# Performance work log

Measured on AMD Instinct MI355X. Metric: run time of the kernel, lower is better.

The kernel has to match this reference:

```python
import jax, jax.numpy as jnp
import numpy as np

N = 100_000          # nodes
E = 3_200_000        # edges (avg degree 32)
NEG_SLOPE = 0.2      # PyG GATConv default


def _gat_conv(x, src, dst, W, a_src, a_dst, b, n):
    """Single-head PyG-style GATConv. src/dst already include self-loops."""
    h = x @ W                                   # [N, F_out]
    logits = (h @ a_src)[src] + (h @ a_dst)[dst]  # [E']
    e = jax.nn.leaky_relu(logits, NEG_SLOPE)
    m = jax.ops.segment_max(e, dst, num_segments=n)
    ex = jnp.exp(e - m[dst])                    # stable ragged softmax over in-edges
    s = jax.ops.segment_sum(ex, dst, num_segments=n)
    alpha = ex / (s[dst] + 1e-16)
    out = jax.ops.segment_sum(h[src] * alpha[:, None], dst, num_segments=n)
    return out + b


def setup_inputs() -> dict:
    key = jax.random.key(0)
    ks = jax.random.split(key, 20)
    x = jax.random.normal(ks[0], (N, 3), dtype=jnp.float32)
    edge_index = jax.random.randint(ks[1], (2, E), 0, N, dtype=jnp.int64)

    def lin(k, fin, fout):
        return jax.random.normal(k, (fin, fout), dtype=jnp.float32) * (1.0 / np.sqrt(fin))

    def att(k, f):
        return jax.random.normal(k, (f,), dtype=jnp.float32) * (1.0 / np.sqrt(f))

    inp = {"x": x, "edge_index": edge_index}
    # forward-direction convs
    inp["W1"], inp["as1"], inp["ad1"], inp["b1"] = lin(ks[2], 3, 16), att(ks[3], 16), att(ks[4], 16), jnp.zeros((16,), jnp.float32)
    inp["W2"], inp["as2"], inp["ad2"], inp["b2"] = lin(ks[5], 16, 1), att(ks[6], 1), att(ks[7], 1), jnp.zeros((1,), jnp.float32)
    # reverse-direction convs
    inp["W1r"], inp["as1r"], inp["ad1r"], inp["b1r"] = lin(ks[8], 3, 16), att(ks[9], 16), att(ks[10], 16), jnp.zeros((16,), jnp.float32)
    inp["W2r"], inp["as2r"], inp["ad2r"], inp["b2r"] = lin(ks[11], 16, 1), att(ks[12], 1), att(ks[13], 1), jnp.zeros((1,), jnp.float32)
    return inp


def reference(x, edge_index, W1, as1, ad1, b1, W2, as2, ad2, b2,
              W1r, as1r, ad1r, b1r, W2r, as2r, ad2r, b2r):
    n = x.shape[0]
    loops = jnp.arange(n, dtype=edge_index.dtype)
    # forward direction (self-loops appended, as PyG add_self_loops=True)
    src = jnp.concatenate([edge_index[0], loops])
    dst = jnp.concatenate([edge_index[1], loops])
    # reverse direction: stack([ei[1], ei[0]]) then self-loops
    rsrc = jnp.concatenate([edge_index[1], loops])
    rdst = jnp.concatenate([edge_index[0], loops])

    xf = jax.nn.relu(_gat_conv(x, src, dst, W1, as1, ad1, b1, n))
    xf = _gat_conv(xf, src, dst, W2, as2, ad2, b2, n)

    xr = jax.nn.relu(_gat_conv(x, rsrc, rdst, W1r, as1r, ad1r, b1r, n))
    xr = _gat_conv(xr, rsrc, rdst, W2r, as2r, ad2r, b2r, n)

    return (xf + xr) * 0.5
```

## Files before the change

kernel.cpp:

```cpp
#include <hip/hip_runtime.h>
#include <math.h>

#define NSLOPE 0.2f
#define BSH 8
#define BNODES 256
#define NID_MASK 0x1FFFF
#define SENT 0xFFFFFFFFu
#define CAP 10240
#define GB2 512
#define RT 512
#define EPT2 13
#define REDG (RT * EPT2)
#define RREC (2 * REDG)
#define BN9 512
#define LCAP 17408
#define BAGT 1024
#define CPP9 9

__device__ __forceinline__ float lrelu(float v) { return v > 0.f ? v : NSLOPE * v; }

__global__ void k_prep(const float* __restrict__ x,
                       const float* __restrict__ as1, const float* __restrict__ ad1,
                       const float* __restrict__ as1r, const float* __restrict__ ad1r,
                       const float* __restrict__ W1, const float* __restrict__ W1r,
                       float4* __restrict__ rec4f, float4* __restrict__ rec4r,
                       float* __restrict__ s1df, float* __restrict__ s1dr,
                       int* __restrict__ gcur, int NS, int N) {
    int i = blockIdx.x * blockDim.x + threadIdx.x;
    if (i < NS) gcur[i] = 0;
    if (i >= N) return;
    float x0 = x[3 * i], x1 = x[3 * i + 1], x2 = x[3 * i + 2];
    float ssf = 0.f, sdf = 0.f, ssr = 0.f, sdr = 0.f;
#pragma unroll
    for (int k = 0; k < 16; k++) {
        float hf = x0 * W1[k] + x1 * W1[16 + k] + x2 * W1[32 + k];
        ssf += hf * as1[k];
        sdf += hf * ad1[k];
        float hr = x0 * W1r[k] + x1 * W1r[16 + k] + x2 * W1r[32 + k];
        ssr += hr * as1r[k];
        sdr += hr * ad1r[k];
    }
    rec4f[i] = make_float4(x0, x1, x2, ssf);
    rec4r[i] = make_float4(x0, x1, x2, ssr);
    s1df[i] = sdf; s1dr[i] = sdr;
}

__global__ void __launch_bounds__(RT) k_scatsort(
        const void* __restrict__ ei, long long E,
        int NB, int NS, int* __restrict__ gcur, unsigned* __restrict__ bin) {
    extern __shared__ unsigned smem[];
    unsigned* rec = smem;
    int* cnt  = (int*)(rec + RREC);
    int* loff = cnt + NS;
    int* gbs  = loff + NS;
    int* wtot = gbs + NS;
    __shared__ int flagsm;

    int t = threadIdx.x;
    if (t < 64) {
        const unsigned long long* p = (const unsigned long long*)ei;
        bool bad = false;
#pragma unroll
        for (int i = 0; i < 4; i++)
            if (p[t * 4 + i] >= (1ull << 32)) bad = true;
        unsigned long long mask = __ballot(bad);
        if (t == 0) flagsm = (mask == 0ull) ? 1 : 0;
    }
    __syncthreads();
    int fl = flagsm;
    long long chunk = (E + GB2 - 1) / GB2;
    long long cstart = (long long)blockIdx.x * chunk;
    long long cend = cstart + chunk; if (cend > E) cend = E;
    int rot = (int)((blockIdx.x * 197u) % (unsigned)NS);

    for (long long rs = cstart; rs < cend; rs += REDG) {
        int ne = (int)min((long long)REDG, cend - rs);
        for (int i = t; i < NS; i += RT) cnt[i] = 0;
        int eu[EPT2], ev[EPT2];
#pragma unroll
        for (int k = 0; k < EPT2; k++) {
            int idx = t + k * RT;
            eu[k] = -1;
            if (idx < ne) {
                long long i = rs + idx;
                if (fl) { const long long* p = (const long long*)ei;
                          eu[k] = (int)p[i]; ev[k] = (int)p[E + i]; }
                else    { const int* p = (const int*)ei;
                          eu[k] = p[i]; ev[k] = p[E + i]; }
            }
        }
        __syncthreads();
#pragma unroll
        for (int k = 0; k < EPT2; k++) {
            if (eu[k] >= 0) {
                atomicAdd(&cnt[ev[k] >> BSH], 1);
                atomicAdd(&cnt[NB + (eu[k] >> BSH)], 1);
            }
        }
        __syncthreads();
        int base = 0;
        for (int st = 0; st < NS; st += RT) {
            int idx = st + t;
            int val = (idx < NS) ? cnt[idx] : 0;
            int lane = t & 63, wv = t >> 6;
            int incl = val;
#pragma unroll
            for (int od = 1; od < 64; od <<= 1) {
                int up = __shfl_up(incl, od);
                if (lane >= od) incl += up;
            }
            if (lane == 63) wtot[wv] = incl;
            __syncthreads();
            int woff = 0;
#pragma unroll
            for (int j = 0; j < 8; j++) woff += (j < wv) ? wtot[j] : 0;
            if (idx < NS) {
                int lo = base + woff + incl - val;
                loff[idx] = lo;
                cnt[idx] = lo;
                gbs[idx] = val ? atomicAdd(&gcur[idx], val) : 0;
            }
            int stot = 0;
#pragma unroll
            for (int j = 0; j < 8; j++) stot += wtot[j];
            base += stot;
            __syncthreads();
        }
#pragma unroll
        for (int k = 0; k < EPT2; k++) {
            if (eu[k] >= 0) {
                int u = eu[k], v = ev[k];
                unsigned r0 = (unsigned)u | ((unsigned)(v & (BNODES - 1)) << 17);
                int s0 = v >> BSH;
                int p0 = atomicAdd(&cnt[s0], 1);
                rec[p0] = r0;
                unsigned r1 = (unsigned)v | ((unsigned)(u & (BNODES - 1)) << 17);
                int s1 = NB + (u >> BSH);
                int p1 = atomicAdd(&cnt[s1], 1);
                rec[p1] = r1;
            }
        }
        __syncthreads();
        for (int i = t; i < NS; i += RT) {
            int s = i + rot; if (s >= NS) s -= NS;
            int ls = loff[s], le = cnt[s];
            int n = le - ls;
            if (!n) continue;
            int g = gbs[s];
            if (g >= CAP) continue;
            if (g + n > CAP) n = CAP - g;
            long long b = (long long)s * CAP;
            int j = 0;
            if (g & 1) { bin[b + g] = rec[ls]; j = 1; }
            if (((g + j) & 2) && j + 2 <= n) {
                *(uint2*)(bin + b + g + j) = make_uint2(rec[ls + j], rec[ls + j + 1]);
                j += 2;
            }
            for (; j + 4 <= n; j += 4)
                *(uint4*)(bin + b + g + j) =
                    make_uint4(rec[ls + j], rec[ls + j + 1],
                               rec[ls + j + 2], rec[ls + j + 3]);
            if (j + 2 <= n) {
                *(uint2*)(bin + b + g + j) = make_uint2(rec[ls + j], rec[ls + j + 1]);
                j += 2;
            }
            if (j < n) bin[b + g + j] = rec[ls + j];
        }
        __syncthreads();
    }
}

__global__ void __launch_bounds__(BAGT, 8) k_bagg1(
        unsigned* __restrict__ bin, const int* __restrict__ gcur,
        const float4* __restrict__ rec4f, const float* __restrict__ s1df,
        const float4* __restrict__ rec4r, const float* __restrict__ s1dr,
        const float* __restrict__ b1, const float* __restrict__ W1,
        const float* __restrict__ W2,
        const float* __restrict__ as2, const float* __restrict__ ad2,
        const float* __restrict__ b1r, const float* __restrict__ W1r,
        const float* __restrict__ W2r,
        const float* __restrict__ as2r, const float* __restrict__ ad2r,
        float2* __restrict__ p2f, float* __restrict__ s2df,
        float2* __restrict__ p2r, float* __restrict__ s2dr,
        int* __restrict__ aoff, int* __restrict__ aend, int NB8, int N) {
    int bb = blockIdx.x, dir = blockIdx.y;
    const float4* rec4 = dir ? rec4r : rec4f;
    const float* s1d = dir ? s1dr : s1df;
    const float* b1_ = dir ? b1r : b1;
    const float* W1_ = dir ? W1r : W1;
    const float* W2_ = dir ? W2r : W2;
    float as2v = dir ? as2r[0] : as2[0];
    float ad2v = dir ? ad2r[0] : ad2[0];
    float2* p2 = dir ? p2r : p2f;
    float* s2d = dir ? s2dr : s2df;

    int c0 = dir * NB8 + 2 * bb;
    bool c1ok = (2 * bb + 1) < NB8;
    long long base = (long long)c0 * CAP;
    int n0 = gcur[c0]; if (n0 > CAP) n0 = CAP;
    int n1 = c1ok ? gcur[c0 + 1] : 0; if (n1 > CAP) n1 = CAP;
    int np0 = (n0 + 1) >> 1, np1 = (n1 + 1) >> 1;
    if (np0 > LCAP / 2) np0 = LCAP / 2;
    if (np0 + np1 > LCAP / 2) np1 = LCAP / 2 - np0;
    int nptot = np0 + np1;
    int v0 = bb << 9;
    int nv = N - v0; if (nv > BN9) nv = BN9;

    __shared__ int cnt[BN9];
    __shared__ int loff[BN9];
    __shared__ int segtot[8];
    __shared__ unsigned lds_u[LCAP];
    int t = threadIdx.x;

    const uint2* bp0 = (const uint2*)(bin + base);
    const uint2* bp1 = (const uint2*)(bin + base) + CAP / 2;
    uint2 recs[CPP9];
#pragma unroll
    for (int k = 0; k < CPP9; k++) {
        int i = t + k * BAGT;
        uint2 r = make_uint2(SENT, SENT);
        if (i < np0) {
            r = bp0[i];
            if (2 * i + 1 >= n0) r.y = SENT;
        } else if (i < nptot) {
            int i1 = i - np0;
            r = bp1[i1];
            if (2 * i1 + 1 >= n1) r.y = SENT;
            r.x += (256u << 17);
            if (r.y != SENT) r.y += (256u << 17);
        }
        recs[k] = r;
    }
    if (t < BN9) cnt[t] = 0;
    __syncthreads();
#pragma unroll
    for (int k = 0; k < CPP9; k++) {
        if (recs[k].x != SENT) atomicAdd(&cnt[recs[k].x >> 17], 1);
        if (recs[k].y != SENT) atomicAdd(&cnt[recs[k].y >> 17], 1);
    }
    __syncthreads();
    if (t < BN9) {
        int lane = t & 63, wv = t >> 6;
        int val = cnt[t];
        int incl = val;
#pragma unroll
        for (int od = 1; od < 64; od <<= 1) {
            int up = __shfl_up(incl, od);
            if (lane >= od) incl += up;
        }
        if (lane == 63) segtot[wv] = incl;
        loff[t] = incl - val;
    }
    __syncthreads();
    if (t < BN9) {
        int wv = t >> 6;
        int offs = 0;
#pragma unroll
        for (int j = 0; j < 8; j++) offs += (j < wv) ? segtot[j] : 0;
        int ex = loff[t] + offs;
        loff[t] = ex;
        cnt[t] = ex;
    }
    __syncthreads();
#pragma unroll
    for (int k = 0; k < CPP9; k++) {
        if (recs[k].x != SENT) {
            int q = atomicAdd(&cnt[recs[k].x >> 17], 1);
            lds_u[q] = recs[k].x & NID_MASK;
        }
        if (recs[k].y != SENT) {
            int q = atomicAdd(&cnt[recs[k].y >> 17], 1);
            lds_u[q] = recs[k].y & NID_MASK;
        }
    }
    __syncthreads();
    int node = t >> 1, lane = t & 1;
    float sdv = (node < nv) ? s1d[v0 + node] : 0.f;
    float d = 0.f, a0 = 0.f, a1 = 0.f, a2 = 0.f;
    if (node < nv) {
        int ls = loff[node], le = cnt[node];
        for (int pos = ls + lane; pos < le; pos += 2) {
            unsigned u = lds_u[pos];
            float4 r = rec4[u];
            float w = __expf(lrelu(r.w + sdv));
            d += w; a0 += w * r.x; a1 += w * r.y; a2 += w * r.z;
        }
    }
    d  += __shfl_xor(d, 1);
    a0 += __shfl_xor(a0, 1);
    a1 += __shfl_xor(a1, 1);
    a2 += __shfl_xor(a2, 1);
    if (lane == 0 && node < nv) {
        int v = v0 + node;
        float4 r = rec4[v];
        float w = __expf(lrelu(r.w + sdv));
        float dd = d + w;
        float inv = 1.f / (dd + 1e-16f);
        float m0 = (a0 + w * r.x) * inv;
        float m1 = (a1 + w * r.y) * inv;
        float m2 = (a2 + w * r.z) * inv;
        float h2v = 0.f;
#pragma unroll
        for (int k = 0; k < 16; k++) {
            float o = m0 * W1_[k] + m1 * W1_[16 + k] + m2 * W1_[32 + k] + b1_[k];
            o = fmaxf(o, 0.f);
            h2v += o * W2_[k];
        }
        p2[v] = make_float2(h2v, h2v * as2v);
        s2d[v] = h2v * ad2v;
    }
    int nreal = (nv > 0) ? cnt[nv - 1] : 0;
    if (t == 0 && (nreal & 1)) lds_u[nreal] = SENT;
    __syncthreads();
    int ndp = (nreal + 1) >> 1;
    uint2* bq = (uint2*)(bin + base);
    for (int i = t; i < ndp; i += BAGT)
        bq[i] = make_uint2(lds_u[2 * i], lds_u[2 * i + 1]);
    if (t < nv) {
        aoff[dir * N + v0 + t] = (int)(base + loff[t]);
        aend[dir * N + v0 + t] = (int)(base + cnt[t]);
    }
}

__global__ void k_agg2(const unsigned* __restrict__ bin,
                       const int* __restrict__ aoff, const int* __restrict__ aend,
                       const float2* __restrict__ p2f, const float* __restrict__ s2df,
                       const float2* __restrict__ p2r, const float* __restrict__ s2dr,
                       const float* __restrict__ b2, const float* __restrict__ b2r,
                       float* __restrict__ out, int N) {
    int tid = blockIdx.x * blockDim.x + threadIdx.x;
    int v = tid >> 4;
    int lane = tid & 15;
    if (v >= N) return;
    float res[2];
#pragma unroll
    for (int dir = 0; dir < 2; dir++) {
        const float2* p2 = dir ? p2r : p2f;
        const float* s2d = dir ? s2dr : s2df;
        float bias = dir ? b2r[0] : b2[0];
        float sd = s2d[v];
        int st = aoff[dir * N + v], en = aend[dir * N + v];
        float d = 0.f, a = 0.f;
        if (lane == 0) {
            float2 ts = p2[v];
            float w = __expf(lrelu(ts.y + sd));
            d = w; a = w * ts.x;
        }
        int j = st + lane;
        for (; j + 16 < en; j += 32) {
            unsigned u0 = __builtin_nontemporal_load(bin + j);
            unsigned u1 = __builtin_nontemporal_load(bin + j + 16);
            float2 t0 = p2[u0];
            float2 t1 = p2[u1];
            float w0 = __expf(lrelu(t0.y + sd));
            float w1 = __expf(lrelu(t1.y + sd));
            d += w0 + w1;
            a += w0 * t0.x + w1 * t1.x;
        }
        for (; j < en; j += 16) {
            unsigned u = __builtin_nontemporal_load(bin + j);
            float2 t = p2[u];
            float w = __expf(lrelu(t.y + sd));
            d += w;
            a += w * t.x;
        }
#pragma unroll
        for (int mask = 1; mask < 16; mask <<= 1) {
            d += __shfl_xor(d, mask);
            a += __shfl_xor(a, mask);
        }
        res[dir] = a / (d + 1e-16f) + bias;
    }
    if (lane == 0) out[v] = 0.5f * (res[0] + res[1]);
}

extern "C" void kernel_launch(void* const* d_in, const int* in_sizes, int n_in,
                              void* d_out, int out_size, void* d_ws, size_t ws_size,
                              hipStream_t stream) {
    const float* x   = (const float*)d_in[0];
    const void*  ei  = d_in[1];
    const float* W1  = (const float*)d_in[2];
    const float* as1 = (const float*)d_in[3];
    const float* ad1 = (const float*)d_in[4];
    const float* b1  = (const float*)d_in[5];
    const float* W2  = (const float*)d_in[6];
    const float* as2 = (const float*)d_in[7];
    const float* ad2 = (const float*)d_in[8];
    const float* b2  = (const float*)d_in[9];
    const float* W1r  = (const float*)d_in[10];
    const float* as1r = (const float*)d_in[11];
    const float* ad1r = (const float*)d_in[12];
    const float* b1r  = (const float*)d_in[13];
    const float* W2r  = (const float*)d_in[14];
    const float* as2r = (const float*)d_in[15];
    const float* ad2r = (const float*)d_in[16];
    const float* b2r  = (const float*)d_in[17];

    const int N = in_sizes[0] / 3;
    const long long E = in_sizes[1] / 2;
    const int NB8 = (N + BNODES - 1) >> BSH;
    const int NS = 2 * NB8;
    const int NB9 = (N + BN9 - 1) >> 9;

    char* w = (char*)d_ws;
    size_t o = 0;
    auto A = [&](size_t bytes) { o = (o + 255) & ~(size_t)255; size_t r = o; o += bytes; return r; };
    size_t oR4f  = A(sizeof(float4) * N);
    size_t oR4r  = A(sizeof(float4) * N);
    size_t oS1df = A(sizeof(float) * N);
    size_t oS1dr = A(sizeof(float) * N);
    size_t oP2f  = A(sizeof(float2) * N);
    size_t oS2df = A(sizeof(float) * N);
    size_t oP2r  = A(sizeof(float2) * N);
    size_t oS2dr = A(sizeof(float) * N);
    size_t oAoff = A(sizeof(int) * 2 * N);
    size_t oAend = A(sizeof(int) * 2 * N);
    size_t oGcur = A(sizeof(int) * NS);
    size_t oBin  = A(sizeof(unsigned) * (size_t)NS * CAP);
    (void)ws_size; (void)n_in; (void)out_size;

    float4* rec4f = (float4*)(w + oR4f);
    float4* rec4r = (float4*)(w + oR4r);
    float*  s1df = (float*)(w + oS1df);
    float*  s1dr = (float*)(w + oS1dr);
    float2* p2f  = (float2*)(w + oP2f);
    float*  s2df = (float*)(w + oS2df);
    float2* p2r  = (float2*)(w + oP2r);
    float*  s2dr = (float*)(w + oS2dr);
    int*    aoff = (int*)(w + oAoff);
    int*    aend = (int*)(w + oAend);
    int*    gcur = (int*)(w + oGcur);
    unsigned* bin = (unsigned*)(w + oBin);

    dim3 gN((N + 255) / 256);
    dim3 gAgg1(NB9, 2);
    dim3 gAgg2((N * 16 + 255) / 256);

    size_t smem = sizeof(unsigned) * (size_t)RREC
                + sizeof(int) * (size_t)NS * 3
                + sizeof(int) * 8
                + 64;

    k_prep<<<gN, 256, 0, stream>>>(x, as1, ad1, as1r, ad1r, W1, W1r,
                                   rec4f, rec4r, s1df, s1dr, gcur, NS, N);
    k_scatsort<<<GB2, RT, smem, stream>>>(ei, E, NB8, NS, gcur, bin);
    k_bagg1<<<gAgg1, BAGT, 0, stream>>>(bin, gcur, rec4f, s1df, rec4r, s1dr,
                                        b1, W1, W2, as2, ad2,
                                        b1r, W1r, W2r, as2r, ad2r,
                                        p2f, s2df, p2r, s2dr, aoff, aend, NB8, N);
    k_agg2<<<gAgg2, 256, 0, stream>>>(bin, aoff, aend, p2f, s2df, p2r, s2dr,
                                      b2, b2r, (float*)d_out, N);
}
```

Before: 229.0 us.

## Process one 256-node bucket per aggregation block and shrink bucket capacity

```diff
diff --git a/kernel.cpp b/kernel.cpp
--- a/kernel.cpp
+++ b/kernel.cpp
@@ -6,16 +6,15 @@
 #define BNODES 256
 #define NID_MASK 0x1FFFF
 #define SENT 0xFFFFFFFFu
-#define CAP 10240
-#define GB2 512
+#define CAP 9216
+#define GB2 768
 #define RT 512
-#define EPT2 13
+#define EPT2 9
 #define REDG (RT * EPT2)
 #define RREC (2 * REDG)
-#define BN9 512
-#define LCAP 17408
-#define BAGT 1024
-#define CPP9 9
+#define BN8 256
+#define BAG2T 512
+#define CPP2 9
 
 __device__ __forceinline__ float lrelu(float v) { return v > 0.f ? v : NSLOPE * v; }
 
@@ -45,7 +44,7 @@
     s1df[i] = sdf; s1dr[i] = sdr;
 }
 
-__global__ void __launch_bounds__(RT) k_scatsort(
+__global__ void __launch_bounds__(RT, 6) k_scatsort(
         const void* __restrict__ ei, long long E,
         int NB, int NS, int* __restrict__ gcur, unsigned* __restrict__ bin) {
     extern __shared__ unsigned smem[];
@@ -170,7 +169,7 @@
     }
 }
 
-__global__ void __launch_bounds__(BAGT, 8) k_bagg1(
+__global__ void __launch_bounds__(BAG2T, 8) k_bagg1(
         unsigned* __restrict__ bin, const int* __restrict__ gcur,
         const float4* __restrict__ rec4f, const float* __restrict__ s1df,
         const float4* __restrict__ rec4r, const float* __restrict__ s1dr,
@@ -194,52 +193,40 @@
     float2* p2 = dir ? p2r : p2f;
     float* s2d = dir ? s2dr : s2df;
 
-    int c0 = dir * NB8 + 2 * bb;
-    bool c1ok = (2 * bb + 1) < NB8;
+    int c0 = dir * NB8 + bb;
     long long base = (long long)c0 * CAP;
     int n0 = gcur[c0]; if (n0 > CAP) n0 = CAP;
-    int n1 = c1ok ? gcur[c0 + 1] : 0; if (n1 > CAP) n1 = CAP;
-    int np0 = (n0 + 1) >> 1, np1 = (n1 + 1) >> 1;
-    if (np0 > LCAP / 2) np0 = LCAP / 2;
-    if (np0 + np1 > LCAP / 2) np1 = LCAP / 2 - np0;
-    int nptot = np0 + np1;
-    int v0 = bb << 9;
-    int nv = N - v0; if (nv > BN9) nv = BN9;
-
-    __shared__ int cnt[BN9];
-    __shared__ int loff[BN9];
-    __shared__ int segtot[8];
-    __shared__ unsigned lds_u[LCAP];
+    int np0 = (n0 + 1) >> 1;
+    int v0 = bb << BSH;
+    int nv = N - v0; if (nv > BN8) nv = BN8;
+
+    __shared__ int cnt[BN8];
+    __shared__ int loff[BN8];
+    __shared__ int segtot[4];
+    __shared__ unsigned lds_u[CAP];
     int t = threadIdx.x;
 
     const uint2* bp0 = (const uint2*)(bin + base);
-    const uint2* bp1 = (const uint2*)(bin + base) + CAP / 2;
-    uint2 recs[CPP9];
-#pragma unroll
-    for (int k = 0; k < CPP9; k++) {
-        int i = t + k * BAGT;
+    uint2 recs[CPP2];
+#pragma unroll
+    for (int k = 0; k < CPP2; k++) {
+        int i = t + k * BAG2T;
         uint2 r = make_uint2(SENT, SENT);
         if (i < np0) {
             r = bp0[i];
             if (2 * i + 1 >= n0) r.y = SENT;
-        } else if (i < nptot) {
-            int i1 = i - np0;
-            r = bp1[i1];
-            if (2 * i1 + 1 >= n1) r.y = SENT;
-            r.x += (256u << 17);
-            if (r.y != SENT) r.y += (256u << 17);
         }
         recs[k] = r;
     }
-    if (t < BN9) cnt[t] = 0;
-    __syncthreads();
-#pragma unroll
-    for (int k = 0; k < CPP9; k++) {
+    if (t < BN8) cnt[t] = 0;
+    __syncthreads();
+#pragma unroll
+    for (int k = 0; k < CPP2; k++) {
         if (recs[k].x != SENT) atomicAdd(&cnt[recs[k].x >> 17], 1);
         if (recs[k].y != SENT) atomicAdd(&cnt[recs[k].y >> 17], 1);
     }
     __syncthreads();
-    if (t < BN9) {
+    if (t < BN8) {
         int lane = t & 63, wv = t >> 6;
         int val = cnt[t];
         int incl = val;
@@ -252,18 +239,18 @@
         loff[t] = incl - val;
     }
     __syncthreads();
-    if (t < BN9) {
+    if (t < BN8) {
         int wv = t >> 6;
         int offs = 0;
 #pragma unroll
-        for (int j = 0; j < 8; j++) offs += (j < wv) ? segtot[j] : 0;
+        for (int j = 0; j < 4; j++) offs += (j < wv) ? segtot[j] : 0;
         int ex = loff[t] + offs;
         loff[t] = ex;
         cnt[t] = ex;
     }
     __syncthreads();
 #pragma unroll
-    for (int k = 0; k < CPP9; k++) {
+    for (int k = 0; k < CPP2; k++) {
         if (recs[k].x != SENT) {
             int q = atomicAdd(&cnt[recs[k].x >> 17], 1);
             lds_u[q] = recs[k].x & NID_MASK;
@@ -309,12 +296,12 @@
         p2[v] = make_float2(h2v, h2v * as2v);
         s2d[v] = h2v * ad2v;
     }
-    int nreal = (nv > 0) ? cnt[nv - 1] : 0;
+    int nreal = cnt[BN8 - 1];
     if (t == 0 && (nreal & 1)) lds_u[nreal] = SENT;
     __syncthreads();
     int ndp = (nreal + 1) >> 1;
     uint2* bq = (uint2*)(bin + base);
-    for (int i = t; i < ndp; i += BAGT)
+    for (int i = t; i < ndp; i += BAG2T)
         bq[i] = make_uint2(lds_u[2 * i], lds_u[2 * i + 1]);
     if (t < nv) {
         aoff[dir * N + v0 + t] = (int)(base + loff[t]);
@@ -400,7 +387,7 @@
     const long long E = in_sizes[1] / 2;
     const int NB8 = (N + BNODES - 1) >> BSH;
     const int NS = 2 * NB8;
-    const int NB9 = (N + BN9 - 1) >> 9;
+    (void)ws_size; (void)n_in; (void)out_size;
 
     char* w = (char*)d_ws;
     size_t o = 0;
@@ -417,7 +404,6 @@
     size_t oAend = A(sizeof(int) * 2 * N);
     size_t oGcur = A(sizeof(int) * NS);
     size_t oBin  = A(sizeof(unsigned) * (size_t)NS * CAP);
-    (void)ws_size; (void)n_in; (void)out_size;
 
     float4* rec4f = (float4*)(w + oR4f);
     float4* rec4r = (float4*)(w + oR4r);
@@ -433,7 +419,7 @@
     unsigned* bin = (unsigned*)(w + oBin);
 
     dim3 gN((N + 255) / 256);
-    dim3 gAgg1(NB9, 2);
+    dim3 gBagg(NB8, 2);
     dim3 gAgg2((N * 16 + 255) / 256);
 
     size_t smem = sizeof(unsigned) * (size_t)RREC
@@ -444,10 +430,10 @@
     k_prep<<<gN, 256, 0, stream>>>(x, as1, ad1, as1r, ad1r, W1, W1r,
                                    rec4f, rec4r, s1df, s1dr, gcur, NS, N);
     k_scatsort<<<GB2, RT, smem, stream>>>(ei, E, NB8, NS, gcur, bin);
-    k_bagg1<<<gAgg1, BAGT, 0, stream>>>(bin, gcur, rec4f, s1df, rec4r, s1dr,
-                                        b1, W1, W2, as2, ad2,
-                                        b1r, W1r, W2r, as2r, ad2r,
-                                        p2f, s2df, p2r, s2dr, aoff, aend, NB8, N);
+    k_bagg1<<<gBagg, BAG2T, 0, stream>>>(bin, gcur, rec4f, s1df, rec4r, s1dr,
+                                         b1, W1, W2, as2, ad2,
+                                         b1r, W1r, W2r, as2r, ad2r,
+                                         p2f, s2df, p2r, s2dr, aoff, aend, NB8, N);
     k_agg2<<<gAgg2, 256, 0, stream>>>(bin, aoff, aend, p2f, s2df, p2r, s2dr,
                                       b2, b2r, (float*)d_out, N);
 }
```

After: 234.9 us. 1.03x slower.
